# Optimization experiments

Hardware: AMD Instinct MI355X
Metric: run time of the kernel (lower is better)

Reference implementation:

```python
import jax, jax.numpy as jnp
import numpy as np

B, C, H, W = 8, 256, 64, 64

def setup_inputs() -> dict:
    key = jax.random.key(0)
    ks = jax.random.split(key, 8)
    s = 0.02  # keep logits in a sane range
    return {
        "x": jax.random.normal(ks[0], (B, C, H, W), jnp.float32),
        "motion_info": jax.random.normal(ks[1], (B, C, H, W), jnp.float32),
        "wq": jax.random.normal(ks[2], (C, C), jnp.float32) * s,
        "bq": jax.random.normal(ks[3], (C,), jnp.float32) * s,
        "wk": jax.random.normal(ks[4], (C, C), jnp.float32) * s,
        "bk": jax.random.normal(ks[5], (C,), jnp.float32) * s,
        "wv": jax.random.normal(ks[6], (C, C), jnp.float32) * s,
        "bv": jax.random.normal(ks[7], (C,), jnp.float32) * s,
    }

def reference(x, motion_info, wq, bq, wk, bk, wv, bv):
    b, c, h, w = x.shape
    n = h * w
    scale = c ** (-0.5)
    # 1x1 convs == channel-mixing GEMMs; flatten spatial to tokens
    xf = x.reshape(b, c, n)              # [B,C,N]
    mf = motion_info.reshape(b, c, n)    # [B,C,N]
    q = jnp.einsum('dc,bcn->bdn', wq, xf) + bq[None, :, None]
    k = jnp.einsum('dc,bcn->bdn', wk, mf) + bk[None, :, None]
    v = jnp.einsum('dc,bcn->bdn', wv, mf) + bv[None, :, None]
    # attn[b,i,j] = <q[:,i], k[:,j]> * scale, softmax over j
    attn = jax.nn.softmax(jnp.einsum('bci,bcj->bij', q, k) * scale, axis=-1)
    # out[b,c,i] = sum_j v[b,c,j] * attn[b,i,j]
    out = jnp.einsum('bcj,bij->bci', v, attn)
    return out.reshape(b, c, h, w)
```

## Files before the change

kernel.cpp:

```cpp
#include <hip/hip_runtime.h>
#include <hip/hip_bf16.h>

#define BATCH 8
#define CH    256
#define NTOK  4096

typedef __bf16 bf16_t;
typedef __bf16 bf16x8 __attribute__((ext_vector_type(8)));
typedef __bf16 bf16x4 __attribute__((ext_vector_type(4)));
typedef float  fx4    __attribute__((ext_vector_type(4)));

#define GLOAD_LDS16(gptr, lptr) \
    __builtin_amdgcn_global_load_lds( \
        (const __attribute__((address_space(1))) void*)(gptr), \
        (__attribute__((address_space(3))) void*)(lptr), 16, 0, 0)


__global__ __launch_bounds__(256) void wcvt_kernel(
    const float* __restrict__ wq, const float* __restrict__ wk,
    const float* __restrict__ wv, bf16_t* __restrict__ wb)
{
    const int mat = blockIdx.y;
    const float* __restrict__ W = (mat == 0) ? wq : (mat == 1 ? wk : wv);
    const int idx = (blockIdx.x * 256 + threadIdx.x) * 4;
    const float4 v = *(const float4*)&W[idx];
    bf16x4 pk;
    pk[0] = (bf16_t)v.x; pk[1] = (bf16_t)v.y;
    pk[2] = (bf16_t)v.z; pk[3] = (bf16_t)v.w;
    *(bf16x4*)&wb[(size_t)mat * 65536 + idx] = pk;
}

__global__ __launch_bounds__(256, 2) void proj_kernel(
    const float* __restrict__ x, const float* __restrict__ motion,
    const bf16_t* __restrict__ wb,
    const float* __restrict__ bq, const float* __restrict__ bk,
    const float* __restrict__ bv,
    bf16_t* __restrict__ qg, bf16_t* __restrict__ kg, bf16_t* __restrict__ vg)
{
    const int b  = blockIdx.x & 7;
    const int n0 = (blockIdx.x >> 3) * 64;

    __shared__ __align__(16) unsigned char smem[70656];
    bf16_t* Xt    = (bf16_t*)smem;
    bf16_t* Mt    = (bf16_t*)(smem + 33792);
    float*  biasL = (float*)(smem + 67584);
    bf16_t* OutQK = (bf16_t*)smem;
    bf16_t* OutV  = (bf16_t*)smem;

    const int tid  = threadIdx.x;
    const int w    = tid >> 6;
    const int lane = tid & 63;
    const int l16  = lane & 15;
    const int quad = lane >> 4;

    biasL[tid]       = bq[tid];
    biasL[tid + 256] = bk[tid];
    biasL[tid + 512] = bv[tid];

    #pragma unroll
    for (int s = 0; s < 2; ++s) {
        const float* __restrict__ src = s ? motion : x;
        bf16_t* dst = s ? Mt : Xt;
        for (int it = 0; it < 16; ++it) {
            const int c  = it * 16 + (tid >> 4);
            const int j4 = (tid & 15) * 4;
            const float4 v = *(const float4*)&src[((size_t)b * CH + c) * NTOK + n0 + j4];
            const int g  = tid & 7;
            const int pc = (((c >> 3) ^ g) << 3) + (c & 7);
            dst[(j4 + 0) * 264 + pc] = (bf16_t)v.x;
            dst[(j4 + 1) * 264 + pc] = (bf16_t)v.y;
            dst[(j4 + 2) * 264 + pc] = (bf16_t)v.z;
            dst[(j4 + 3) * 264 + pc] = (bf16_t)v.w;
        }
    }
    __syncthreads();

    bf16x8 ax[8], am[8];
    {
        const int g = (4 * w + (l16 >> 2)) & 7;
        const bf16_t* xr = Xt + (w * 16 + l16) * 264;
        const bf16_t* mr = Mt + (w * 16 + l16) * 264;
        #pragma unroll
        for (int cs = 0; cs < 8; ++cs) {
            const int off = ((cs * 4 + quad) ^ g) << 3;
            ax[cs] = *(const bf16x8*)(xr + off);
            am[cs] = *(const bf16x8*)(mr + off);
        }
    }
    __syncthreads();

    fx4 acc[16];

    auto gemm = [&](const bf16x8* af, const bf16_t* __restrict__ Wm) {
        #pragma unroll
        for (int i = 0; i < 16; ++i) acc[i] = (fx4){0.f, 0.f, 0.f, 0.f};
        #pragma unroll
        for (int dp = 0; dp < 16; ++dp) {
            const bf16_t* wr = Wm + ((size_t)(dp * 16 + l16) << 8) + quad * 8;
            bf16x8 bfr[8];
            #pragma unroll
            for (int cs = 0; cs < 8; ++cs)
                bfr[cs] = *(const bf16x8*)(wr + cs * 32);
            #pragma unroll
            for (int cs = 0; cs < 8; ++cs)
                acc[dp] = __builtin_amdgcn_mfma_f32_16x16x32_bf16(af[cs], bfr[cs], acc[dp], 0, 0, 0);
        }
    };

    gemm(ax, wb);
    #pragma unroll
    for (int dp = 0; dp < 16; ++dp) {
        const int d = dp * 16 + l16;
        const float bb = biasL[d];
        #pragma unroll
        for (int r = 0; r < 4; ++r)
            OutQK[(w * 16 + quad * 4 + r) * 264 + d] = (bf16_t)((acc[dp][r] + bb) * 0.0625f);
    }
    __syncthreads();
    #pragma unroll
    for (int it = 0; it < 8; ++it) {
        const int n  = it * 8 + (tid >> 5);
        const int d8 = (tid & 31) * 8;
        const bf16x8 vv = *(const bf16x8*)&OutQK[n * 264 + d8];
        *(bf16x8*)&qg[((size_t)b * NTOK + n0 + n) * CH + d8] = vv;
    }

    gemm(am, wb + 65536);
    __syncthreads();
    #pragma unroll
    for (int dp = 0; dp < 16; ++dp) {
        const int d = dp * 16 + l16;
        const float bb = biasL[256 + d];
        #pragma unroll
        for (int r = 0; r < 4; ++r)
            OutQK[(w * 16 + quad * 4 + r) * 264 + d] = (bf16_t)(acc[dp][r] + bb);
    }
    __syncthreads();
    #pragma unroll
    for (int it = 0; it < 8; ++it) {
        const int n  = it * 8 + (tid >> 5);
        const int d8 = (tid & 31) * 8;
        const bf16x8 vv = *(const bf16x8*)&OutQK[n * 264 + d8];
        *(bf16x8*)&kg[((size_t)b * NTOK + n0 + n) * CH + d8] = vv;
    }

    gemm(am, wb + 131072);
    __syncthreads();
    #pragma unroll
    for (int dp = 0; dp < 16; ++dp) {
        const int d = dp * 16 + l16;
        const float bb = biasL[512 + d];
        bf16x4 pk;
        #pragma unroll
        for (int r = 0; r < 4; ++r)
            pk[r] = (bf16_t)(acc[dp][r] + bb);
        *(bf16x4*)&OutV[d * 72 + w * 16 + quad * 4] = pk;
    }
    __syncthreads();
    #pragma unroll
    for (int it = 0; it < 8; ++it) {
        const int d  = it * 32 + (tid >> 3);
        const int n8 = (tid & 7) * 8;
        const bf16x8 vv = *(const bf16x8*)&OutV[d * 72 + n8];
        *(bf16x8*)&vg[((size_t)b * CH + d) * NTOK + n0 + n8] = vv;
    }
}

__global__ __launch_bounds__(256, 2) void attn_kernel(
    const bf16_t* __restrict__ qg, const bf16_t* __restrict__ kg,
    const bf16_t* __restrict__ vg, float* __restrict__ out)
{
    const int b  = blockIdx.x & 7;
    const int i0 = (blockIdx.x >> 3) * 64;

    __shared__ __align__(16) unsigned char smem[71168];
    bf16_t* const K0   = (bf16_t*)smem;
    bf16_t* const K1   = (bf16_t*)(smem + 16384);
    bf16_t* const V0   = (bf16_t*)(smem + 32768);
    bf16_t* const V1   = (bf16_t*)(smem + 49152);
    bf16_t* const P    = (bf16_t*)(smem + 65536);
    float*  const lred = (float*)(smem + 70656);

    const int tid  = threadIdx.x;
    const int w    = tid >> 6;
    const int lane = tid & 63;
    const int l16  = lane & 15;
    const int quad = lane >> 4;
    const int ih   = w & 1;
    const int jh   = w >> 1;
    const int ch   = w & 1;
    const int is2  = w >> 1;
    const int w4   = w * 4;

    bf16x8 qf[2][8];
    #pragma unroll
    for (int isub = 0; isub < 2; ++isub) {
        const bf16_t* qb = qg + ((size_t)b * NTOK + i0 + ih * 32 + isub * 16 + l16) * CH;
        #pragma unroll
        for (int cs = 0; cs < 8; ++cs)
            qf[isub][cs] = *(const bf16x8*)(qb + cs * 32 + quad * 8);
    }

    fx4 oacc[8][2];
    #pragma unroll
    for (int i = 0; i < 8; ++i) {
        oacc[i][0] = (fx4){0.f, 0.f, 0.f, 0.f};
        oacc[i][1] = (fx4){0.f, 0.f, 0.f, 0.f};
    }
    float rs0[4] = {0.f, 0.f, 0.f, 0.f};
    float rs1[4] = {0.f, 0.f, 0.f, 0.f};

    const int jrow = jh * 16 + l16;
    const int sxk  = l16 & 7;
    const int svo  = (quad ^ ((l16 >> 1) & 3)) * 8;
    const int vsl  = (lane & 3) ^ ((lane >> 3) & 3);

    auto stageK = [&](bf16_t* Kb, int t) {
        const int j0 = t * 32;
        #pragma unroll
        for (int it = 0; it < 4; ++it) {
            const int N   = w4 + it;
            const int kj  = 2 * N + (lane >> 5);
            const int ksl = (lane & 31) ^ (kj & 7);
            GLOAD_LDS16(kg + (((size_t)b * NTOK + j0 + kj) << 8) + ksl * 8, Kb + N * 512);
        }
    };
    auto stageV = [&](bf16_t* Vb, int t) {
        const int j0 = t * 32;
        #pragma unroll
        for (int it = 0; it < 4; ++it) {
            const int N  = w4 + it;
            const int vc = N * 16 + (lane >> 2);
            GLOAD_LDS16(vg + (((size_t)b * CH + vc) << 12) + j0 + vsl * 8, Vb + N * 512);
        }
    };

    stageK(K0, 0);
    stageV(V0, 0);

    auto tile = [&](bf16_t* const Kc, bf16_t* const Kn,
                    bf16_t* const Vc, bf16_t* const Vn,
                    const int t, const bool last) {
        if (!last) stageK(Kn, t + 1);
        if (!last) { asm volatile("s_waitcnt vmcnt(8)" ::: "memory"); }
        else       { asm volatile("s_waitcnt vmcnt(4)" ::: "memory"); }
        __builtin_amdgcn_s_barrier();
        __builtin_amdgcn_sched_barrier(0);
        if (!last) stageV(Vn, t + 1);

        fx4 s0 = (fx4){0.f, 0.f, 0.f, 0.f};
        fx4 s1 = (fx4){0.f, 0.f, 0.f, 0.f};
        {
            const bf16_t* krow = Kc + jrow * 256;
            __builtin_amdgcn_s_setprio(1);
            #pragma unroll
            for (int cs = 0; cs < 8; ++cs) {
                const bf16x8 kf = *(const bf16x8*)(krow + (((cs * 4 + quad) ^ sxk) * 8));
                s0 = __builtin_amdgcn_mfma_f32_16x16x32_bf16(qf[0][cs], kf, s0, 0, 0, 0);
                s1 = __builtin_amdgcn_mfma_f32_16x16x32_bf16(qf[1][cs], kf, s1, 0, 0, 0);
            }
            __builtin_amdgcn_s_setprio(0);
        }
        {
            bf16_t* prow = P + (ih * 32 + quad * 4) * 40 + jh * 16 + (l16 & ~1);
            #pragma unroll
            for (int r = 0; r < 4; ++r) {
                const float p0 = __expf(s0[r]);
                const float p1 = __expf(s1[r]);
                rs0[r] += p0;
                rs1[r] += p1;
                const float n0f = __shfl_xor(p0, 1);
                const float n1f = __shfl_xor(p1, 1);
                unsigned int pk0, pk1;
                asm("v_cvt_pk_bf16_f32 %0, %1, %2" : "=v"(pk0) : "v"(p0), "v"(n0f));
                asm("v_cvt_pk_bf16_f32 %0, %1, %2" : "=v"(pk1) : "v"(p1), "v"(n1f));
                if (!(l16 & 1)) {
                    *(unsigned int*)(prow + r * 40)       = pk0;
                    *(unsigned int*)(prow + r * 40 + 640) = pk1;
                }
            }
        }
        if (!last) { asm volatile("s_waitcnt vmcnt(8) lgkmcnt(0)" ::: "memory"); }
        else       { asm volatile("s_waitcnt vmcnt(0) lgkmcnt(0)" ::: "memory"); }
        __builtin_amdgcn_s_barrier();
        __builtin_amdgcn_sched_barrier(0);

        {
            const bf16x8 pf0 = *(const bf16x8*)(P + (is2 * 32 + l16) * 40 + quad * 8);
            const bf16x8 pf1 = *(const bf16x8*)(P + (is2 * 32 + 16 + l16) * 40 + quad * 8);
            const bf16_t* vbase = Vc + (ch * 128 + l16) * 32 + svo;
            __builtin_amdgcn_s_setprio(1);
            #pragma unroll
            for (int cp8 = 0; cp8 < 8; ++cp8) {
                const bf16x8 vf = *(const bf16x8*)(vbase + cp8 * 512);
                oacc[cp8][0] = __builtin_amdgcn_mfma_f32_16x16x32_bf16(vf, pf0, oacc[cp8][0], 0, 0, 0);
                oacc[cp8][1] = __builtin_amdgcn_mfma_f32_16x16x32_bf16(vf, pf1, oacc[cp8][1], 0, 0, 0);
            }
            __builtin_amdgcn_s_setprio(0);
        }
    };

    #pragma unroll 1
    for (int t = 0; t < 126; t += 2) {
        tile(K0, K1, V0, V1, t,     false);
        tile(K1, K0, V1, V0, t + 1, false);
    }
    tile(K0, K1, V0, V1, 126, false);
    tile(K1, K0, V1, V0, 127, true);

    #pragma unroll
    for (int r = 0; r < 4; ++r) {
        float v0 = rs0[r], v1 = rs1[r];
        v0 += __shfl_xor(v0, 1); v0 += __shfl_xor(v0, 2);
        v0 += __shfl_xor(v0, 4); v0 += __shfl_xor(v0, 8);
        v1 += __shfl_xor(v1, 1); v1 += __shfl_xor(v1, 2);
        v1 += __shfl_xor(v1, 4); v1 += __shfl_xor(v1, 8);
        rs0[r] = v0; rs1[r] = v1;
    }
    __syncthreads();
    if (l16 == 0) {
        #pragma unroll
        for (int r = 0; r < 4; ++r) {
            lred[jh * 64 + ih * 32 + quad * 4 + r]      = rs0[r];
            lred[jh * 64 + ih * 32 + 16 + quad * 4 + r] = rs1[r];
        }
    }
    __syncthreads();

    const int   row0  = is2 * 32 + l16;
    const float linv0 = 1.0f / (lred[row0] + lred[64 + row0]);
    const float linv1 = 1.0f / (lred[row0 + 16] + lred[64 + row0 + 16]);

    const size_t obase = (size_t)b * CH * NTOK + i0 + is2 * 32 + l16;
    #pragma unroll
    for (int cp8 = 0; cp8 < 8; ++cp8) {
        const int c0 = (ch * 8 + cp8) * 16 + quad * 4;
        #pragma unroll
        for (int r = 0; r < 4; ++r) {
            out[obase + (size_t)(c0 + r) * NTOK]      = oacc[cp8][0][r] * linv0;
            out[obase + (size_t)(c0 + r) * NTOK + 16] = oacc[cp8][1][r] * linv1;
        }
    }
}

extern "C" void kernel_launch(void* const* d_in, const int* in_sizes, int n_in,
                              void* d_out, int out_size, void* d_ws, size_t ws_size,
                              hipStream_t stream) {
    const float* x  = (const float*)d_in[0];
    const float* mi = (const float*)d_in[1];
    const float* wq = (const float*)d_in[2];
    const float* bq = (const float*)d_in[3];
    const float* wk = (const float*)d_in[4];
    const float* bk = (const float*)d_in[5];
    const float* wv = (const float*)d_in[6];
    const float* bv = (const float*)d_in[7];

    bf16_t* qg = (bf16_t*)d_ws;
    bf16_t* kg = qg + (size_t)BATCH * NTOK * CH;
    bf16_t* vg = kg + (size_t)BATCH * NTOK * CH;
    bf16_t* wb = (bf16_t*)d_out;

    dim3 wgrid(64, 3);
    wcvt_kernel<<<wgrid, 256, 0, stream>>>(wq, wk, wv, wb);

    proj_kernel<<<BATCH * (NTOK / 64), 256, 0, stream>>>(x, mi, wb, bq, bk, bv, qg, kg, vg);

    attn_kernel<<<BATCH * (NTOK / 64), 256, 0, stream>>>(qg, kg, vg, (float*)d_out);
}
```

Measured before the change: 378.4 us.

## Load V fragments directly from global into registers and widen key tile to 64

The attention kernel no longer stages V through LDS. Each wave now owns 64 output channels and loads its V fragments from global memory straight into registers, while K tiles double to 64 keys per iteration so there are half as many barriers and loop trips. The aim is to cut LDS traffic and synchronisation per tile. In exchange, V is read from global without LDS sharing, register pressure rises with 16 accumulators plus 8 V fragments, and LDS use grows slightly, which may hurt occupancy at 2 blocks per CU.

```diff
diff --git a/kernel.cpp b/kernel.cpp
--- a/kernel.cpp
+++ b/kernel.cpp
@@ -173,13 +173,11 @@
     const int b  = blockIdx.x & 7;
     const int i0 = (blockIdx.x >> 3) * 64;
 
-    __shared__ __align__(16) unsigned char smem[71168];
+    __shared__ __align__(16) unsigned char smem[75264];
     bf16_t* const K0   = (bf16_t*)smem;
-    bf16_t* const K1   = (bf16_t*)(smem + 16384);
-    bf16_t* const V0   = (bf16_t*)(smem + 32768);
-    bf16_t* const V1   = (bf16_t*)(smem + 49152);
+    bf16_t* const K1   = (bf16_t*)(smem + 32768);
     bf16_t* const P    = (bf16_t*)(smem + 65536);
-    float*  const lred = (float*)(smem + 70656);
+    float*  const lred = (float*)(smem + 74752);
 
     const int tid  = threadIdx.x;
     const int w    = tid >> 6;
@@ -188,9 +186,8 @@
     const int quad = lane >> 4;
     const int ih   = w & 1;
     const int jh   = w >> 1;
-    const int ch   = w & 1;
-    const int is2  = w >> 1;
-    const int w4   = w * 4;
+    const int cq   = w;
+    const int w8   = w * 8;
 
     bf16x8 qf[2][8];
     #pragma unroll
@@ -201,72 +198,74 @@
             qf[isub][cs] = *(const bf16x8*)(qb + cs * 32 + quad * 8);
     }
 
-    fx4 oacc[8][2];
-    #pragma unroll
-    for (int i = 0; i < 8; ++i) {
-        oacc[i][0] = (fx4){0.f, 0.f, 0.f, 0.f};
-        oacc[i][1] = (fx4){0.f, 0.f, 0.f, 0.f};
-    }
+    fx4 oacc[4][4];
+    #pragma unroll
+    for (int i = 0; i < 4; ++i)
+        #pragma unroll
+        for (int j = 0; j < 4; ++j) oacc[i][j] = (fx4){0.f, 0.f, 0.f, 0.f};
     float rs0[4] = {0.f, 0.f, 0.f, 0.f};
     float rs1[4] = {0.f, 0.f, 0.f, 0.f};
 
-    const int jrow = jh * 16 + l16;
-    const int sxk  = l16 & 7;
-    const int svo  = (quad ^ ((l16 >> 1) & 3)) * 8;
-    const int vsl  = (lane & 3) ^ ((lane >> 3) & 3);
+    const int sxk = l16 & 7;
+    const bf16_t* const vbase =
+        vg + ((size_t)b * CH + cq * 64 + l16) * NTOK + quad * 8;
 
     auto stageK = [&](bf16_t* Kb, int t) {
-        const int j0 = t * 32;
-        #pragma unroll
-        for (int it = 0; it < 4; ++it) {
-            const int N   = w4 + it;
+        const int j0 = t * 64;
+        #pragma unroll
+        for (int it = 0; it < 8; ++it) {
+            const int N   = w8 + it;
             const int kj  = 2 * N + (lane >> 5);
             const int ksl = (lane & 31) ^ (kj & 7);
-            GLOAD_LDS16(kg + (((size_t)b * NTOK + j0 + kj) << 8) + ksl * 8, Kb + N * 512);
+            GLOAD_LDS16(kg + (((size_t)b * NTOK + j0 + kj) << 8) + ksl * 8,
+                        Kb + N * 512);
         }
     };
-    auto stageV = [&](bf16_t* Vb, int t) {
-        const int j0 = t * 32;
-        #pragma unroll
-        for (int it = 0; it < 4; ++it) {
-            const int N  = w4 + it;
-            const int vc = N * 16 + (lane >> 2);
-            GLOAD_LDS16(vg + (((size_t)b * CH + vc) << 12) + j0 + vsl * 8, Vb + N * 512);
-        }
-    };
 
     stageK(K0, 0);
-    stageV(V0, 0);
-
-    auto tile = [&](bf16_t* const Kc, bf16_t* const Kn,
-                    bf16_t* const Vc, bf16_t* const Vn,
-                    const int t, const bool last) {
+
+    auto tile = [&](bf16_t* const Kc, bf16_t* const Kn, const int t, const bool last) {
+        const int j0 = t * 64;
+
+        bf16x8 vf0[4], vf1[4];
+        #pragma unroll
+        for (int cp = 0; cp < 4; ++cp) {
+            vf0[cp] = *(const bf16x8*)(vbase + (size_t)(cp * 16) * NTOK + j0);
+            vf1[cp] = *(const bf16x8*)(vbase + (size_t)(cp * 16) * NTOK + j0 + 32);
+        }
         if (!last) stageK(Kn, t + 1);
-        if (!last) { asm volatile("s_waitcnt vmcnt(8)" ::: "memory"); }
-        else       { asm volatile("s_waitcnt vmcnt(4)" ::: "memory"); }
+        if (!last) { asm volatile("s_waitcnt vmcnt(16)" ::: "memory"); }
+        else       { asm volatile("s_waitcnt vmcnt(8)"  ::: "memory"); }
         __builtin_amdgcn_s_barrier();
-        __builtin_amdgcn_sched_barrier(0);
-        if (!last) stageV(Vn, t + 1);
-
-        fx4 s0 = (fx4){0.f, 0.f, 0.f, 0.f};
-        fx4 s1 = (fx4){0.f, 0.f, 0.f, 0.f};
+        asm volatile("" ::: "memory");
+
+        fx4 s00 = (fx4){0.f,0.f,0.f,0.f}, s01 = (fx4){0.f,0.f,0.f,0.f};
+        fx4 s10 = (fx4){0.f,0.f,0.f,0.f}, s11 = (fx4){0.f,0.f,0.f,0.f};
         {
-            const bf16_t* krow = Kc + jrow * 256;
             __builtin_amdgcn_s_setprio(1);
+            const bf16_t* krow0 = Kc + (jh * 32 + l16) * 256;
+            const bf16_t* krow1 = krow0 + 16 * 256;
             #pragma unroll
             for (int cs = 0; cs < 8; ++cs) {
-                const bf16x8 kf = *(const bf16x8*)(krow + (((cs * 4 + quad) ^ sxk) * 8));
-                s0 = __builtin_amdgcn_mfma_f32_16x16x32_bf16(qf[0][cs], kf, s0, 0, 0, 0);
-                s1 = __builtin_amdgcn_mfma_f32_16x16x32_bf16(qf[1][cs], kf, s1, 0, 0, 0);
+                const int co = ((cs * 4 + quad) ^ sxk) << 3;
+                const bf16x8 kf0 = *(const bf16x8*)(krow0 + co);
+                const bf16x8 kf1 = *(const bf16x8*)(krow1 + co);
+                s00 = __builtin_amdgcn_mfma_f32_16x16x32_bf16(qf[0][cs], kf0, s00, 0, 0, 0);
+                s10 = __builtin_amdgcn_mfma_f32_16x16x32_bf16(qf[1][cs], kf0, s10, 0, 0, 0);
+                s01 = __builtin_amdgcn_mfma_f32_16x16x32_bf16(qf[0][cs], kf1, s01, 0, 0, 0);
+                s11 = __builtin_amdgcn_mfma_f32_16x16x32_bf16(qf[1][cs], kf1, s11, 0, 0, 0);
             }
             __builtin_amdgcn_s_setprio(0);
         }
-        {
-            bf16_t* prow = P + (ih * 32 + quad * 4) * 40 + jh * 16 + (l16 & ~1);
+        #pragma unroll
+        for (int jp = 0; jp < 2; ++jp) {
+            const fx4 sa = jp ? s01 : s00;
+            const fx4 sb = jp ? s11 : s10;
+            bf16_t* prow = P + (ih * 32 + quad * 4) * 72 + jh * 32 + jp * 16 + (l16 & ~1);
             #pragma unroll
             for (int r = 0; r < 4; ++r) {
-                const float p0 = __expf(s0[r]);
-                const float p1 = __expf(s1[r]);
+                const float p0 = __expf(sa[r]);
+                const float p1 = __expf(sb[r]);
                 rs0[r] += p0;
                 rs1[r] += p1;
                 const float n0f = __shfl_xor(p0, 1);
@@ -275,38 +274,39 @@
                 asm("v_cvt_pk_bf16_f32 %0, %1, %2" : "=v"(pk0) : "v"(p0), "v"(n0f));
                 asm("v_cvt_pk_bf16_f32 %0, %1, %2" : "=v"(pk1) : "v"(p1), "v"(n1f));
                 if (!(l16 & 1)) {
-                    *(unsigned int*)(prow + r * 40)       = pk0;
-                    *(unsigned int*)(prow + r * 40 + 640) = pk1;
+                    *(unsigned int*)(prow + r * 72)            = pk0;
+                    *(unsigned int*)(prow + r * 72 + 16 * 72)  = pk1;
                 }
             }
         }
-        if (!last) { asm volatile("s_waitcnt vmcnt(8) lgkmcnt(0)" ::: "memory"); }
-        else       { asm volatile("s_waitcnt vmcnt(0) lgkmcnt(0)" ::: "memory"); }
+        asm volatile("s_waitcnt lgkmcnt(0)" ::: "memory");
         __builtin_amdgcn_s_barrier();
-        __builtin_amdgcn_sched_barrier(0);
+        asm volatile("" ::: "memory");
 
         {
-            const bf16x8 pf0 = *(const bf16x8*)(P + (is2 * 32 + l16) * 40 + quad * 8);
-            const bf16x8 pf1 = *(const bf16x8*)(P + (is2 * 32 + 16 + l16) * 40 + quad * 8);
-            const bf16_t* vbase = Vc + (ch * 128 + l16) * 32 + svo;
             __builtin_amdgcn_s_setprio(1);
             #pragma unroll
-            for (int cp8 = 0; cp8 < 8; ++cp8) {
-                const bf16x8 vf = *(const bf16x8*)(vbase + cp8 * 512);
-                oacc[cp8][0] = __builtin_amdgcn_mfma_f32_16x16x32_bf16(vf, pf0, oacc[cp8][0], 0, 0, 0);
-                oacc[cp8][1] = __builtin_amdgcn_mfma_f32_16x16x32_bf16(vf, pf1, oacc[cp8][1], 0, 0, 0);
+            for (int is = 0; is < 4; ++is) {
+                const bf16_t* pr = P + (is * 16 + l16) * 72 + quad * 8;
+                const bf16x8 pf0 = *(const bf16x8*)(pr);
+                const bf16x8 pf1 = *(const bf16x8*)(pr + 32);
+                #pragma unroll
+                for (int cp = 0; cp < 4; ++cp) {
+                    oacc[cp][is] = __builtin_amdgcn_mfma_f32_16x16x32_bf16(vf0[cp], pf0, oacc[cp][is], 0, 0, 0);
+                    oacc[cp][is] = __builtin_amdgcn_mfma_f32_16x16x32_bf16(vf1[cp], pf1, oacc[cp][is], 0, 0, 0);
+                }
             }
             __builtin_amdgcn_s_setprio(0);
         }
     };
 
     #pragma unroll 1
-    for (int t = 0; t < 126; t += 2) {
-        tile(K0, K1, V0, V1, t,     false);
-        tile(K1, K0, V1, V0, t + 1, false);
-    }
-    tile(K0, K1, V0, V1, 126, false);
-    tile(K1, K0, V1, V0, 127, true);
+    for (int t = 0; t < 62; t += 2) {
+        tile(K0, K1, t,     false);
+        tile(K1, K0, t + 1, false);
+    }
+    tile(K0, K1, 62, false);
+    tile(K1, K0, 63, true);
 
     #pragma unroll
     for (int r = 0; r < 4; ++r) {
@@ -327,18 +327,23 @@
     }
     __syncthreads();
 
-    const int   row0  = is2 * 32 + l16;
-    const float linv0 = 1.0f / (lred[row0] + lred[64 + row0]);
-    const float linv1 = 1.0f / (lred[row0 + 16] + lred[64 + row0 + 16]);
-
-    const size_t obase = (size_t)b * CH * NTOK + i0 + is2 * 32 + l16;
-    #pragma unroll
-    for (int cp8 = 0; cp8 < 8; ++cp8) {
-        const int c0 = (ch * 8 + cp8) * 16 + quad * 4;
-        #pragma unroll
-        for (int r = 0; r < 4; ++r) {
-            out[obase + (size_t)(c0 + r) * NTOK]      = oacc[cp8][0][r] * linv0;
-            out[obase + (size_t)(c0 + r) * NTOK + 16] = oacc[cp8][1][r] * linv1;
+    float linv[4];
+    #pragma unroll
+    for (int is = 0; is < 4; ++is) {
+        const int row = is * 16 + l16;
+        linv[is] = 1.0f / (lred[row] + lred[64 + row]);
+    }
+
+    const size_t obase = ((size_t)b * CH + cq * 64) * NTOK + i0 + l16;
+    #pragma unroll
+    for (int cp = 0; cp < 4; ++cp) {
+        #pragma unroll
+        for (int is = 0; is < 4; ++is) {
+            #pragma unroll
+            for (int r = 0; r < 4; ++r) {
+                out[obase + (size_t)(cp * 16 + quad * 4 + r) * NTOK + is * 16] =
+                    oacc[cp][is][r] * linv[is];
+            }
         }
     }
 }
```

After: 491.7 us. 1.3x slower.
